# Kernel optimization log

Hardware: AMD Instinct MI355X
Metric: run time of the kernel (lower is better)

The kernel has to match this reference:

```python
import jax, jax.numpy as jnp
import numpy as np

N, F_IN, UNITS, HEADS = 4096, 128, 64, 4
EDGE_P = 0.01  # adjacency density


def setup_inputs() -> dict:
    key = jax.random.key(0)
    k1, k2, k3, k4, k5 = jax.random.split(key, 5)
    inputs = jax.random.normal(k1, (N, F_IN), dtype=jnp.float32)
    adj = jax.random.bernoulli(k2, EDGE_P, (N, N)).astype(jnp.float32)
    # glorot-normal-ish parameter scales
    w = jax.random.normal(k3, (F_IN, UNITS), dtype=jnp.float32) * np.float32(np.sqrt(2.0 / (F_IN + UNITS)))
    attn_w1 = jax.random.normal(k4, (UNITS, HEADS), dtype=jnp.float32) * np.float32(np.sqrt(2.0 / (UNITS + HEADS)))
    attn_w2 = jax.random.normal(k5, (UNITS, HEADS), dtype=jnp.float32) * np.float32(np.sqrt(2.0 / (UNITS + HEADS)))
    return {"inputs": inputs, "adj": adj, "w": w, "attn_w1": attn_w1, "attn_w2": attn_w2}


def reference(inputs, adj, w, attn_w1, attn_w2):
    # dropout=0, bias=0, final_layer=False, activation=relu
    x = inputs @ w                                  # [N, U]
    e1 = x @ attn_w1                                # [N, H]
    e2 = x @ attn_w2                                # [N, H]
    # coeffs[i, j, h] = relu(e1[i, h] + e2[j, h])
    coeffs = jax.nn.relu(e1[:, None, :] + e2[None, :, :])   # [N, N, H]
    # NOTE: original multiplies by adj (zeros -> logit 0, not -inf) then softmax over j
    scores = adj[:, :, None] * coeffs               # [N, N, H]
    attn = jax.nn.softmax(scores, axis=1)           # normalize over neighbors j
    # per-head aggregation, concat heads -> [N, H*U] (head-major blocks)
    out = jnp.einsum("ijh,ju->ihu", attn, x).reshape(N, HEADS * UNITS)
    return jax.nn.relu(out)
```

## Files before the change

### kernel.cpp

```cpp
#include <hip/hip_runtime.h>
#include <hip/hip_bf16.h>

#define N_NODES 4096
#define F_IN    128
#define UNITS   64
#define HEADS   4
#define WT_PITCH 132
#define CHUNK   64

__global__ __launch_bounds__(256) void k1(const float* __restrict__ inputs,
                                          const float* __restrict__ w,
                                          const float* __restrict__ aw1,
                                          const float* __restrict__ aw2,
                                          float* __restrict__ x,
                                          float* __restrict__ e1,
                                          float* __restrict__ e2,
                                          float* __restrict__ partial) {
    __shared__ float w_t[UNITS * WT_PITCH];
    __shared__ float in_lds[16 * F_IN];
    __shared__ float x_lds[16 * 65];
    __shared__ float aw_lds[2 * UNITS * HEADS];

    const int t = threadIdx.x;
    const int b = blockIdx.x;
    const int row0 = b * 16;

    for (int idx = t; idx < F_IN * UNITS; idx += 256) {
        const int u = idx & 63;
        const int k = idx >> 6;
        w_t[u * WT_PITCH + k] = w[idx];
    }
    {
        const float4* src = (const float4*)(inputs + (size_t)row0 * F_IN);
        float4* dst = (float4*)in_lds;
        for (int idx = t; idx < 16 * F_IN / 4; idx += 256) dst[idx] = src[idx];
    }
    if (t < UNITS * HEADS) {
        aw_lds[t] = aw1[t];
        aw_lds[UNITS * HEADS + t] = aw2[t];
    }
    __syncthreads();

    const int u = t & 63;
    const int rg = t >> 6;
    float acc0 = 0.f, acc1 = 0.f, acc2 = 0.f, acc3 = 0.f;
    const float4* wrow = (const float4*)(w_t + u * WT_PITCH);
    const float4* i0 = (const float4*)(in_lds + (rg * 4 + 0) * F_IN);
    const float4* i1 = (const float4*)(in_lds + (rg * 4 + 1) * F_IN);
    const float4* i2 = (const float4*)(in_lds + (rg * 4 + 2) * F_IN);
    const float4* i3 = (const float4*)(in_lds + (rg * 4 + 3) * F_IN);
#pragma unroll 8
    for (int c = 0; c < F_IN / 4; c++) {
        const float4 wv = wrow[c];
        float4 v;
        v = i0[c]; acc0 = fmaf(wv.x, v.x, fmaf(wv.y, v.y, fmaf(wv.z, v.z, fmaf(wv.w, v.w, acc0))));
        v = i1[c]; acc1 = fmaf(wv.x, v.x, fmaf(wv.y, v.y, fmaf(wv.z, v.z, fmaf(wv.w, v.w, acc1))));
        v = i2[c]; acc2 = fmaf(wv.x, v.x, fmaf(wv.y, v.y, fmaf(wv.z, v.z, fmaf(wv.w, v.w, acc2))));
        v = i3[c]; acc3 = fmaf(wv.x, v.x, fmaf(wv.y, v.y, fmaf(wv.z, v.z, fmaf(wv.w, v.w, acc3))));
    }
    x_lds[(rg * 4 + 0) * 65 + u] = acc0;
    x_lds[(rg * 4 + 1) * 65 + u] = acc1;
    x_lds[(rg * 4 + 2) * 65 + u] = acc2;
    x_lds[(rg * 4 + 3) * 65 + u] = acc3;
    x[(size_t)(row0 + rg * 4 + 0) * UNITS + u] = acc0;
    x[(size_t)(row0 + rg * 4 + 1) * UNITS + u] = acc1;
    x[(size_t)(row0 + rg * 4 + 2) * UNITS + u] = acc2;
    x[(size_t)(row0 + rg * 4 + 3) * UNITS + u] = acc3;
    __syncthreads();

    if (t < 128) {
        const int r = t >> 3;
        const int rem = t & 7;
        const int h = rem & 3;
        const bool first = rem < 4;
        const float* aw = aw_lds + (first ? 0 : UNITS * HEADS);
        float s = 0.f;
#pragma unroll 8
        for (int uu = 0; uu < UNITS; uu++)
            s += x_lds[r * 65 + uu] * aw[uu * HEADS + h];
        (first ? e1 : e2)[(size_t)(row0 + r) * HEADS + h] = s;
    }

    if (t < 64) {
        float s = 0.f;
#pragma unroll
        for (int r = 0; r < 16; r++) s += x_lds[r * 65 + t];
        partial[b * 64 + t] = s;
    }
}

__global__ __launch_bounds__(256) void k1b(const float* __restrict__ partial,
                                           float* __restrict__ S) {
    __shared__ float red[4][64];
    const int u = threadIdx.x & 63;
    const int q = threadIdx.x >> 6;
    float s = 0.f;
#pragma unroll 8
    for (int b = q; b < 256; b += 4) s += partial[b * 64 + u];
    red[q][u] = s;
    __syncthreads();
    if (threadIdx.x < 64) S[u] = red[0][u] + red[1][u] + red[2][u] + red[3][u];
}

__global__ __launch_bounds__(256) void k2(const float* __restrict__ adj,
                                          const float* __restrict__ x,
                                          const float* __restrict__ e1,
                                          const float* __restrict__ e2,
                                          const float* __restrict__ S,
                                          float* __restrict__ out) {
    __shared__ unsigned short nbr[N_NODES];
    __shared__ float xs[CHUNK * UNITS];
    __shared__ float wgt[CHUNK * 4];
    __shared__ int cnt;

    const int i = blockIdx.x;
    const int t = threadIdx.x;

    if (t == 0) cnt = 0;
    __syncthreads();

    const float4* arow = (const float4*)(adj + (size_t)i * N_NODES);
    const float4 v0 = arow[t];
    const float4 v1 = arow[t + 256];
    const float4 v2 = arow[t + 512];
    const float4 v3 = arow[t + 768];
    {
        const int b0 = t * 4;
        if (v0.x != 0.f) nbr[atomicAdd(&cnt, 1)] = (unsigned short)(b0 + 0);
        if (v0.y != 0.f) nbr[atomicAdd(&cnt, 1)] = (unsigned short)(b0 + 1);
        if (v0.z != 0.f) nbr[atomicAdd(&cnt, 1)] = (unsigned short)(b0 + 2);
        if (v0.w != 0.f) nbr[atomicAdd(&cnt, 1)] = (unsigned short)(b0 + 3);
        const int b1 = (t + 256) * 4;
        if (v1.x != 0.f) nbr[atomicAdd(&cnt, 1)] = (unsigned short)(b1 + 0);
        if (v1.y != 0.f) nbr[atomicAdd(&cnt, 1)] = (unsigned short)(b1 + 1);
        if (v1.z != 0.f) nbr[atomicAdd(&cnt, 1)] = (unsigned short)(b1 + 2);
        if (v1.w != 0.f) nbr[atomicAdd(&cnt, 1)] = (unsigned short)(b1 + 3);
        const int b2 = (t + 512) * 4;
        if (v2.x != 0.f) nbr[atomicAdd(&cnt, 1)] = (unsigned short)(b2 + 0);
        if (v2.y != 0.f) nbr[atomicAdd(&cnt, 1)] = (unsigned short)(b2 + 1);
        if (v2.z != 0.f) nbr[atomicAdd(&cnt, 1)] = (unsigned short)(b2 + 2);
        if (v2.w != 0.f) nbr[atomicAdd(&cnt, 1)] = (unsigned short)(b2 + 3);
        const int b3 = (t + 768) * 4;
        if (v3.x != 0.f) nbr[atomicAdd(&cnt, 1)] = (unsigned short)(b3 + 0);
        if (v3.y != 0.f) nbr[atomicAdd(&cnt, 1)] = (unsigned short)(b3 + 1);
        if (v3.z != 0.f) nbr[atomicAdd(&cnt, 1)] = (unsigned short)(b3 + 2);
        if (v3.w != 0.f) nbr[atomicAdd(&cnt, 1)] = (unsigned short)(b3 + 3);
    }
    __syncthreads();

    const int n = cnt;
    const int h = t >> 6;
    const int u = t & 63;

    const float4 e1v = *(const float4*)(e1 + (size_t)i * HEADS);

    float acc = 0.f;
    float den = 0.f;

    for (int base = 0; base < n; base += CHUNK) {
        const int m = min(n - base, CHUNK);

        if (t < m) {
            const int j = nbr[base + t];
            const float4 e2v = *(const float4*)(e2 + (size_t)j * HEADS);
            float4 wv;
            wv.x = __expf(fmaxf(e1v.x + e2v.x, 0.f)) - 1.f;
            wv.y = __expf(fmaxf(e1v.y + e2v.y, 0.f)) - 1.f;
            wv.z = __expf(fmaxf(e1v.z + e2v.z, 0.f)) - 1.f;
            wv.w = __expf(fmaxf(e1v.w + e2v.w, 0.f)) - 1.f;
            *(float4*)(wgt + t * 4) = wv;
        }
        for (int idx = t; idx < m * UNITS; idx += 256) {
            const int k = idx >> 6;
            const int uu = idx & 63;
            xs[idx] = x[(size_t)nbr[base + k] * UNITS + uu];
        }
        __syncthreads();

#pragma unroll 8
        for (int k = 0; k < m; k++) {
            const float wv = wgt[k * 4 + h];
            den += wv;
            acc = fmaf(wv, xs[k * UNITS + u], acc);
        }
        __syncthreads();
    }

    const float numer = S[u] + acc;
    const float denom = (float)N_NODES + den;
    out[(size_t)i * (HEADS * UNITS) + t] = fmaxf(numer / denom, 0.f);
}

extern "C" void kernel_launch(void* const* d_in, const int* in_sizes, int n_in,
                              void* d_out, int out_size, void* d_ws, size_t ws_size,
                              hipStream_t stream) {
    const float* inputs = (const float*)d_in[0];
    const float* adj    = (const float*)d_in[1];
    const float* w      = (const float*)d_in[2];
    const float* aw1    = (const float*)d_in[3];
    const float* aw2    = (const float*)d_in[4];
    float* out = (float*)d_out;

    float* ws = (float*)d_ws;
    float* x       = ws;
    float* e1      = ws + 262144;
    float* e2      = ws + 262144 + 16384;
    float* partial = ws + 262144 + 2 * 16384;
    float* S       = ws + 262144 + 3 * 16384;

    k1<<<256, 256, 0, stream>>>(inputs, w, aw1, aw2, x, e1, e2, partial);
    k1b<<<1, 256, 0, stream>>>(partial, S);
    k2<<<N_NODES, 256, 0, stream>>>(adj, x, e1, e2, S, out);
}
```

Baseline: 118.5 us.

## Use wave ballots for neighbor compaction and per-wave aggregation without block barriers

Neighbor compaction in k2 now uses per-wave ballots and popcounts with one LDS atomic per wave, replacing one atomic per nonzero. The aggregation loop drops the shared x staging and the block barriers. Each wave (one head) computes its own weights, passes (j, weight) pairs through wave-private LDS, reads x rows straight from global/L2, and reduces the denominator with shuffles. k1 also loads w without transposing it, reading it column-wise from LDS. The trade-off is that each head's wave now reloads the same x rows from global memory instead of sharing one LDS copy.

```diff
diff --git a/kernel.cpp b/kernel.cpp
--- a/kernel.cpp
+++ b/kernel.cpp
@@ -5,8 +5,6 @@
 #define F_IN    128
 #define UNITS   64
 #define HEADS   4
-#define WT_PITCH 132
-#define CHUNK   64
 
 __global__ __launch_bounds__(256) void k1(const float* __restrict__ inputs,
                                           const float* __restrict__ w,
@@ -16,7 +14,7 @@
                                           float* __restrict__ e1,
                                           float* __restrict__ e2,
                                           float* __restrict__ partial) {
-    __shared__ float w_t[UNITS * WT_PITCH];
+    __shared__ float w_lds[F_IN * UNITS];
     __shared__ float in_lds[16 * F_IN];
     __shared__ float x_lds[16 * 65];
     __shared__ float aw_lds[2 * UNITS * HEADS];
@@ -25,10 +23,10 @@
     const int b = blockIdx.x;
     const int row0 = b * 16;
 
-    for (int idx = t; idx < F_IN * UNITS; idx += 256) {
-        const int u = idx & 63;
-        const int k = idx >> 6;
-        w_t[u * WT_PITCH + k] = w[idx];
+    {
+        const float4* src = (const float4*)w;
+        float4* dst = (float4*)w_lds;
+        for (int idx = t; idx < F_IN * UNITS / 4; idx += 256) dst[idx] = src[idx];
     }
     {
         const float4* src = (const float4*)(inputs + (size_t)row0 * F_IN);
@@ -44,19 +42,22 @@
     const int u = t & 63;
     const int rg = t >> 6;
     float acc0 = 0.f, acc1 = 0.f, acc2 = 0.f, acc3 = 0.f;
-    const float4* wrow = (const float4*)(w_t + u * WT_PITCH);
-    const float4* i0 = (const float4*)(in_lds + (rg * 4 + 0) * F_IN);
-    const float4* i1 = (const float4*)(in_lds + (rg * 4 + 1) * F_IN);
-    const float4* i2 = (const float4*)(in_lds + (rg * 4 + 2) * F_IN);
-    const float4* i3 = (const float4*)(in_lds + (rg * 4 + 3) * F_IN);
+    const float4* r0 = (const float4*)(in_lds + (rg * 4 + 0) * F_IN);
+    const float4* r1 = (const float4*)(in_lds + (rg * 4 + 1) * F_IN);
+    const float4* r2 = (const float4*)(in_lds + (rg * 4 + 2) * F_IN);
+    const float4* r3 = (const float4*)(in_lds + (rg * 4 + 3) * F_IN);
 #pragma unroll 8
     for (int c = 0; c < F_IN / 4; c++) {
-        const float4 wv = wrow[c];
-        float4 v;
-        v = i0[c]; acc0 = fmaf(wv.x, v.x, fmaf(wv.y, v.y, fmaf(wv.z, v.z, fmaf(wv.w, v.w, acc0))));
-        v = i1[c]; acc1 = fmaf(wv.x, v.x, fmaf(wv.y, v.y, fmaf(wv.z, v.z, fmaf(wv.w, v.w, acc1))));
-        v = i2[c]; acc2 = fmaf(wv.x, v.x, fmaf(wv.y, v.y, fmaf(wv.z, v.z, fmaf(wv.w, v.w, acc2))));
-        v = i3[c]; acc3 = fmaf(wv.x, v.x, fmaf(wv.y, v.y, fmaf(wv.z, v.z, fmaf(wv.w, v.w, acc3))));
+        const int k4 = c * 4;
+        const float w0 = w_lds[(k4 + 0) * UNITS + u];
+        const float w1 = w_lds[(k4 + 1) * UNITS + u];
+        const float w2 = w_lds[(k4 + 2) * UNITS + u];
+        const float w3 = w_lds[(k4 + 3) * UNITS + u];
+        float4 a;
+        a = r0[c]; acc0 = fmaf(a.w, w3, fmaf(a.z, w2, fmaf(a.y, w1, fmaf(a.x, w0, acc0))));
+        a = r1[c]; acc1 = fmaf(a.w, w3, fmaf(a.z, w2, fmaf(a.y, w1, fmaf(a.x, w0, acc1))));
+        a = r2[c]; acc2 = fmaf(a.w, w3, fmaf(a.z, w2, fmaf(a.y, w1, fmaf(a.x, w0, acc2))));
+        a = r3[c]; acc3 = fmaf(a.w, w3, fmaf(a.z, w2, fmaf(a.y, w1, fmaf(a.x, w0, acc3))));
     }
     x_lds[(rg * 4 + 0) * 65 + u] = acc0;
     x_lds[(rg * 4 + 1) * 65 + u] = acc1;
@@ -109,12 +110,13 @@
                                           const float* __restrict__ S,
                                           float* __restrict__ out) {
     __shared__ unsigned short nbr[N_NODES];
-    __shared__ float xs[CHUNK * UNITS];
-    __shared__ float wgt[CHUNK * 4];
+    __shared__ float2 pairs[HEADS][64];
     __shared__ int cnt;
 
     const int i = blockIdx.x;
     const int t = threadIdx.x;
+    const int lane = t & 63;
+    const int h = t >> 6;
 
     if (t == 0) cnt = 0;
     __syncthreads();
@@ -124,69 +126,91 @@
     const float4 v1 = arow[t + 256];
     const float4 v2 = arow[t + 512];
     const float4 v3 = arow[t + 768];
+
+    const unsigned long long b0  = __ballot(v0.x != 0.f);
+    const unsigned long long b1  = __ballot(v0.y != 0.f);
+    const unsigned long long b2  = __ballot(v0.z != 0.f);
+    const unsigned long long b3  = __ballot(v0.w != 0.f);
+    const unsigned long long b4  = __ballot(v1.x != 0.f);
+    const unsigned long long b5  = __ballot(v1.y != 0.f);
+    const unsigned long long b6  = __ballot(v1.z != 0.f);
+    const unsigned long long b7  = __ballot(v1.w != 0.f);
+    const unsigned long long b8  = __ballot(v2.x != 0.f);
+    const unsigned long long b9  = __ballot(v2.y != 0.f);
+    const unsigned long long b10 = __ballot(v2.z != 0.f);
+    const unsigned long long b11 = __ballot(v2.w != 0.f);
+    const unsigned long long b12 = __ballot(v3.x != 0.f);
+    const unsigned long long b13 = __ballot(v3.y != 0.f);
+    const unsigned long long b14 = __ballot(v3.z != 0.f);
+    const unsigned long long b15 = __ballot(v3.w != 0.f);
+
+    const int tot = __popcll(b0) + __popcll(b1) + __popcll(b2) + __popcll(b3)
+                  + __popcll(b4) + __popcll(b5) + __popcll(b6) + __popcll(b7)
+                  + __popcll(b8) + __popcll(b9) + __popcll(b10) + __popcll(b11)
+                  + __popcll(b12) + __popcll(b13) + __popcll(b14) + __popcll(b15);
+
+    int wbase = 0;
+    if (lane == 0) wbase = atomicAdd(&cnt, tot);
+    wbase = __shfl(wbase, 0);
+
+    const unsigned long long lt = (1ull << lane) - 1ull;
     {
-        const int b0 = t * 4;
-        if (v0.x != 0.f) nbr[atomicAdd(&cnt, 1)] = (unsigned short)(b0 + 0);
-        if (v0.y != 0.f) nbr[atomicAdd(&cnt, 1)] = (unsigned short)(b0 + 1);
-        if (v0.z != 0.f) nbr[atomicAdd(&cnt, 1)] = (unsigned short)(b0 + 2);
-        if (v0.w != 0.f) nbr[atomicAdd(&cnt, 1)] = (unsigned short)(b0 + 3);
-        const int b1 = (t + 256) * 4;
-        if (v1.x != 0.f) nbr[atomicAdd(&cnt, 1)] = (unsigned short)(b1 + 0);
-        if (v1.y != 0.f) nbr[atomicAdd(&cnt, 1)] = (unsigned short)(b1 + 1);
-        if (v1.z != 0.f) nbr[atomicAdd(&cnt, 1)] = (unsigned short)(b1 + 2);
-        if (v1.w != 0.f) nbr[atomicAdd(&cnt, 1)] = (unsigned short)(b1 + 3);
-        const int b2 = (t + 512) * 4;
-        if (v2.x != 0.f) nbr[atomicAdd(&cnt, 1)] = (unsigned short)(b2 + 0);
-        if (v2.y != 0.f) nbr[atomicAdd(&cnt, 1)] = (unsigned short)(b2 + 1);
-        if (v2.z != 0.f) nbr[atomicAdd(&cnt, 1)] = (unsigned short)(b2 + 2);
-        if (v2.w != 0.f) nbr[atomicAdd(&cnt, 1)] = (unsigned short)(b2 + 3);
-        const int b3 = (t + 768) * 4;
-        if (v3.x != 0.f) nbr[atomicAdd(&cnt, 1)] = (unsigned short)(b3 + 0);
-        if (v3.y != 0.f) nbr[atomicAdd(&cnt, 1)] = (unsigned short)(b3 + 1);
-        if (v3.z != 0.f) nbr[atomicAdd(&cnt, 1)] = (unsigned short)(b3 + 2);
-        if (v3.w != 0.f) nbr[atomicAdd(&cnt, 1)] = (unsigned short)(b3 + 3);
+        int off = wbase;
+        const int g0 = t * 4, g1 = (t + 256) * 4, g2 = (t + 512) * 4, g3 = (t + 768) * 4;
+        if (v0.x != 0.f) nbr[off + __popcll(b0  & lt)] = (unsigned short)(g0 + 0); off += __popcll(b0);
+        if (v0.y != 0.f) nbr[off + __popcll(b1  & lt)] = (unsigned short)(g0 + 1); off += __popcll(b1);
+        if (v0.z != 0.f) nbr[off + __popcll(b2  & lt)] = (unsigned short)(g0 + 2); off += __popcll(b2);
+        if (v0.w != 0.f) nbr[off + __popcll(b3  & lt)] = (unsigned short)(g0 + 3); off += __popcll(b3);
+        if (v1.x != 0.f) nbr[off + __popcll(b4  & lt)] = (unsigned short)(g1 + 0); off += __popcll(b4);
+        if (v1.y != 0.f) nbr[off + __popcll(b5  & lt)] = (unsigned short)(g1 + 1); off += __popcll(b5);
+        if (v1.z != 0.f) nbr[off + __popcll(b6  & lt)] = (unsigned short)(g1 + 2); off += __popcll(b6);
+        if (v1.w != 0.f) nbr[off + __popcll(b7  & lt)] = (unsigned short)(g1 + 3); off += __popcll(b7);
+        if (v2.x != 0.f) nbr[off + __popcll(b8  & lt)] = (unsigned short)(g2 + 0); off += __popcll(b8);
+        if (v2.y != 0.f) nbr[off + __popcll(b9  & lt)] = (unsigned short)(g2 + 1); off += __popcll(b9);
+        if (v2.z != 0.f) nbr[off + __popcll(b10 & lt)] = (unsigned short)(g2 + 2); off += __popcll(b10);
+        if (v2.w != 0.f) nbr[off + __popcll(b11 & lt)] = (unsigned short)(g2 + 3); off += __popcll(b11);
+        if (v3.x != 0.f) nbr[off + __popcll(b12 & lt)] = (unsigned short)(g3 + 0); off += __popcll(b12);
+        if (v3.y != 0.f) nbr[off + __popcll(b13 & lt)] = (unsigned short)(g3 + 1); off += __popcll(b13);
+        if (v3.z != 0.f) nbr[off + __popcll(b14 & lt)] = (unsigned short)(g3 + 2); off += __popcll(b14);
+        if (v3.w != 0.f) nbr[off + __popcll(b15 & lt)] = (unsigned short)(g3 + 3); off += __popcll(b15);
     }
     __syncthreads();
 
     const int n = cnt;
-    const int h = t >> 6;
-    const int u = t & 63;
-
-    const float4 e1v = *(const float4*)(e1 + (size_t)i * HEADS);
+    const float e1h = e1[(size_t)i * HEADS + h];
 
     float acc = 0.f;
-    float den = 0.f;
-
-    for (int base = 0; base < n; base += CHUNK) {
-        const int m = min(n - base, CHUNK);
-
-        if (t < m) {
-            const int j = nbr[base + t];
-            const float4 e2v = *(const float4*)(e2 + (size_t)j * HEADS);
-            float4 wv;
-            wv.x = __expf(fmaxf(e1v.x + e2v.x, 0.f)) - 1.f;
-            wv.y = __expf(fmaxf(e1v.y + e2v.y, 0.f)) - 1.f;
-            wv.z = __expf(fmaxf(e1v.z + e2v.z, 0.f)) - 1.f;
-            wv.w = __expf(fmaxf(e1v.w + e2v.w, 0.f)) - 1.f;
-            *(float4*)(wgt + t * 4) = wv;
+    float den_lane = 0.f;
+
+    for (int base = 0; base < n; base += 64) {
+        const int m = min(n - base, 64);
+        int j = 0;
+        float wv = 0.f;
+        if (lane < m) {
+            j = nbr[base + lane];
+            const float e2h = e2[(size_t)j * HEADS + h];
+            wv = __expf(fmaxf(e1h + e2h, 0.f)) - 1.f;
+            den_lane += wv;
         }
-        for (int idx = t; idx < m * UNITS; idx += 256) {
-            const int k = idx >> 6;
-            const int uu = idx & 63;
-            xs[idx] = x[(size_t)nbr[base + k] * UNITS + uu];
+        pairs[h][lane] = make_float2(__int_as_float(j), wv);
+
+#pragma unroll 4
+        for (int k = 0; k < m; k++) {
+            const float2 p = pairs[h][k];
+            const int jk = __float_as_int(p.x);
+            acc = fmaf(p.y, x[(jk << 6) + lane], acc);
         }
-        __syncthreads();
-
-#pragma unroll 8
-        for (int k = 0; k < m; k++) {
-            const float wv = wgt[k * 4 + h];
-            den += wv;
-            acc = fmaf(wv, xs[k * UNITS + u], acc);
-        }
-        __syncthreads();
-    }
-
-    const float numer = S[u] + acc;
+    }
+
+    float den = den_lane;
+    den += __shfl_xor(den, 32);
+    den += __shfl_xor(den, 16);
+    den += __shfl_xor(den, 8);
+    den += __shfl_xor(den, 4);
+    den += __shfl_xor(den, 2);
+    den += __shfl_xor(den, 1);
+
+    const float numer = S[lane] + acc;
     const float denom = (float)N_NODES + den;
     out[(size_t)i * (HEADS * UNITS) + t] = fmaxf(numer / denom, 0.f);
 }
```

Result: no change. 119.9 us (+1.3%).
